# Optimization experiments

Measured on AMD Instinct MI355X. Metric: run time of the kernel, lower is better.

## Reference

```python
import jax, jax.numpy as jnp
import numpy as np

NUM_CHUNKS = 8
TOP_K = 2
IN_F = 4096
HID_F = 4096
OUT_F = 4096
B = 4096


def setup_inputs() -> dict:
    key = jax.random.key(0)
    k = jax.random.split(key, 5)
    cin = IN_F // NUM_CHUNKS    # 512
    cout = HID_F // NUM_CHUNKS  # 512
    s_in = 1.0 / np.sqrt(cin)
    s_fin = 1.0 / np.sqrt(cout * TOP_K)
    return {
        "x": jax.random.normal(k[0], (B, IN_F), dtype=jnp.float32),
        # stacked chunk-expert Linear params: y = x @ W + b
        "W_chunks": jax.random.uniform(k[1], (NUM_CHUNKS, cin, cout), jnp.float32, -s_in, s_in),
        "b_chunks": jax.random.uniform(k[2], (NUM_CHUNKS, cout), jnp.float32, -s_in, s_in),
        "W_final": jax.random.uniform(k[3], (cout * TOP_K, OUT_F), jnp.float32, -s_fin, s_fin),
        "b_final": jax.random.uniform(k[4], (OUT_F,), jnp.float32, -s_fin, s_fin),
    }


def reference(x, W_chunks, b_chunks, W_final, b_final):
    Bsz = x.shape[0]
    # split into chunks along feature dim: (B, num_chunks, chunk_in)
    xr = x.reshape(Bsz, NUM_CHUNKS, -1)
    # per-chunk activity = mean(|chunk|) over the whole batch (matches torch .abs().mean())
    activities = jnp.mean(jnp.abs(xr), axis=(0, 2))  # (num_chunks,)
    _, topk_idx = jax.lax.top_k(activities, TOP_K)    # descending, like torch.topk
    # gather selected chunks and their expert weights, run small GEMMs
    x_sel = xr[:, topk_idx, :]                        # (B, k, chunk_in)
    h = jnp.einsum('bkc,kcd->bkd', x_sel, W_chunks[topk_idx]) + b_chunks[topk_idx]
    h = h.reshape(Bsz, -1)                            # concat along feature dim
    out = h @ W_final + b_final                       # (B, out_features)
    return out
```

## Files before the change

kernel.cpp:

```cpp
#include <hip/hip_runtime.h>


typedef __bf16 bf16x8_t __attribute__((ext_vector_type(8)));
typedef float  f32x4_t  __attribute__((ext_vector_type(4)));
typedef unsigned short u16x4 __attribute__((ext_vector_type(4)));

__device__ inline unsigned short f2bf(float f) {
    __bf16 b = (__bf16)f;
    return __builtin_bit_cast(unsigned short, b);
}

__device__ inline void stage_glds(const unsigned short* gtile, int stride, int row0,
                                  unsigned short* lds, int lane) {
    const int r8 = lane >> 3;
    const int gg = (lane & 7) ^ r8;
    const unsigned short* gp = gtile + (size_t)(row0 + r8) * stride + gg * 8;
    unsigned short* lp = lds + row0 * 64;
    __builtin_amdgcn_global_load_lds((const __attribute__((address_space(1))) void*)gp,
                                     (__attribute__((address_space(3))) void*)lp,
                                     16, 0, 0);
}

__device__ inline bf16x8_t ldsfrag(const unsigned short* Ls, int row, int kb) {
    return *(const bf16x8_t*)(Ls + row * 64 + (((kb >> 3) ^ (row & 7)) * 8));
}

__global__ void fused_prep_kernel(const float* __restrict__ x, const float* __restrict__ Wc,
                                  const float* __restrict__ Wf, float* __restrict__ part,
                                  unsigned short* __restrict__ wct, unsigned short* __restrict__ wft) {
    const int b = blockIdx.x;
    const int tid = threadIdx.x;

    if (b < 512) {
        const int chunk = b & 7;
        const int rg = b >> 3;
        const int colf4 = tid & 127;
        const int rsub = tid >> 7;
        const float4* base = (const float4*)x + (size_t)chunk * 128 + colf4;
        float s = 0.f;
        #pragma unroll 4
        for (int i = 0; i < 32; ++i) {
            int row = rg * 64 + i * 2 + rsub;
            float4 v = base[(size_t)row * 1024];
            s += fabsf(v.x) + fabsf(v.y) + fabsf(v.z) + fabsf(v.w);
        }
        #pragma unroll
        for (int off = 32; off > 0; off >>= 1) s += __shfl_down(s, off, 64);
        __shared__ float wsum[4];
        if ((tid & 63) == 0) wsum[tid >> 6] = s;
        __syncthreads();
        if (tid == 0) part[chunk * 64 + rg] = wsum[0] + wsum[1] + wsum[2] + wsum[3];
        return;
    }

    __shared__ float tile[32][33];
    const int tx = tid & 31, ty = tid >> 5;
    const float* src; unsigned short* dst; int R, C, cb, rb;
    int jj = b - 512;
    if (jj < 4096) {
        src = Wf; dst = wft; R = 1024; C = 4096;
        cb = (jj & 127) * 32; rb = (jj >> 7) * 32;
    } else {
        jj -= 4096;
        int c = jj >> 8, t = jj & 255;
        src = Wc + (size_t)c * 262144;
        dst = wct + (size_t)c * 262144;
        R = 512; C = 512;
        cb = (t & 15) * 32; rb = (t >> 4) * 32;
    }
    #pragma unroll
    for (int i = 0; i < 4; ++i)
        tile[ty + i * 8][tx] = src[(size_t)(rb + ty + i * 8) * C + cb + tx];
    __syncthreads();
    {
        const int tx8  = tid & 7;
        const int ty32 = tid >> 3;
        u16x4 hv;
        #pragma unroll
        for (int j = 0; j < 4; ++j) hv[j] = f2bf(tile[tx8 * 4 + j][ty32]);
        *(u16x4*)(dst + (size_t)(cb + ty32) * R + rb + tx8 * 4) = hv;
    }
}

__global__ __launch_bounds__(256, 4)
void gemm1_kernel(const float* __restrict__ x, const unsigned short* __restrict__ wct,
                  const float* __restrict__ bc, const float* __restrict__ part,
                  unsigned short* __restrict__ h) {
    __shared__ __align__(16) unsigned char lds_raw[24576];
    unsigned short* As = (unsigned short*)lds_raw;
    unsigned short* Bs = (unsigned short*)(lds_raw + 8192);

    const int tid = threadIdx.x;
    const int wave = tid >> 6;
    const int lane = tid & 63;

    {
        float* sred = (float*)lds_raw;
        sred[tid] = part[tid];
        sred[tid + 256] = part[tid + 256];
        __syncthreads();
        float* act8 = (float*)(lds_raw + 2048);
        if (tid < 8) {
            float a = 0.f;
            #pragma unroll
            for (int k = 0; k < 64; ++k) a += sred[tid * 64 + k];
            act8[tid] = a;
        }
        __syncthreads();
    }
    int sel0, sel1;
    {
        const float* act8 = (const float*)(lds_raw + 2048);
        float v0 = -1e30f, v1 = -1e30f; int b0 = 0, b1 = 0;
        #pragma unroll
        for (int i = 0; i < 8; ++i) {
            float v = act8[i];
            if (v > v0) { v1 = v0; b1 = b0; v0 = v; b0 = i; }
            else if (v > v1) { v1 = v; b1 = i; }
        }
        sel0 = b0; sel1 = b1;
    }
    __syncthreads();

    const int z = blockIdx.z;
    const int idxz = z ? sel1 : sel0;
    const int m0 = blockIdx.x * 64;
    const int n0 = blockIdx.y * 128;
    const int wm = (wave >> 1) * 32;
    const int wn = (wave & 1) * 64;
    const int rl = lane & 15;
    const int quad = lane >> 4;

    const float* xtile = x + (size_t)m0 * 4096 + idxz * 512;
    const unsigned short* Btile = wct + (size_t)idxz * 262144 + (size_t)n0 * 512;

    f32x4_t acc[4][2] = {};
    const int ar = tid >> 2;
    const int aq = tid & 3;

    for (int k0 = 0; k0 < 512; k0 += 64) {
        #pragma unroll
        for (int s = wave; s < 16; s += 4)
            stage_glds(Btile + k0, 512, s * 8, Bs, lane);
        const float* gr = xtile + (size_t)ar * 4096 + k0;
        #pragma unroll
        for (int j = 0; j < 2; ++j) {
            int gg = aq * 2 + j;
            float4 a = *(const float4*)(gr + gg * 8);
            float4 c = *(const float4*)(gr + gg * 8 + 4);
            bf16x8_t v;
            v[0] = (__bf16)a.x; v[1] = (__bf16)a.y; v[2] = (__bf16)a.z; v[3] = (__bf16)a.w;
            v[4] = (__bf16)c.x; v[5] = (__bf16)c.y; v[6] = (__bf16)c.z; v[7] = (__bf16)c.w;
            *(bf16x8_t*)(As + ar * 64 + ((gg ^ (ar & 7)) * 8)) = v;
        }
        __syncthreads();
        #pragma unroll
        for (int kq = 0; kq < 2; ++kq) {
            const int kb = kq * 32 + quad * 8;
            bf16x8_t af[2], bfr[4];
            #pragma unroll
            for (int i = 0; i < 2; ++i) af[i]  = ldsfrag(As, wm + i * 16 + rl, kb);
            #pragma unroll
            for (int i = 0; i < 4; ++i) bfr[i] = ldsfrag(Bs, wn + i * 16 + rl, kb);
            #pragma unroll
            for (int ni = 0; ni < 4; ++ni)
                #pragma unroll
                for (int mi = 0; mi < 2; ++mi)
                    acc[ni][mi] = __builtin_amdgcn_mfma_f32_16x16x32_bf16(bfr[ni], af[mi], acc[ni][mi], 0, 0, 0);
        }
        __syncthreads();
    }

    const float* bias = bc + (size_t)idxz * 512;
    #pragma unroll
    for (int ni = 0; ni < 4; ++ni) {
        const int colb = n0 + wn + ni * 16 + quad * 4;
        f32x4_t bv4 = *(const f32x4_t*)(bias + colb);
        #pragma unroll
        for (int mi = 0; mi < 2; ++mi) {
            int row = m0 + wm + mi * 16 + rl;
            f32x4_t o = acc[ni][mi] + bv4;
            u16x4 hv;
            #pragma unroll
            for (int j = 0; j < 4; ++j) hv[j] = f2bf(o[j]);
            *(u16x4*)(h + (size_t)row * 1024 + z * 512 + colb) = hv;
        }
    }
}

__global__ __launch_bounds__(256, 4)
void gemm2_kernel(const unsigned short* __restrict__ h, const unsigned short* __restrict__ wft,
                  const float* __restrict__ bfin, float* __restrict__ out) {
    __shared__ __align__(16) unsigned short As[128 * 64];
    __shared__ __align__(16) unsigned short Bs[128 * 64];
    const int m0 = blockIdx.x * 128;
    const int n0 = blockIdx.y * 128;
    const int tid = threadIdx.x;
    const int wave = tid >> 6;
    const int lane = tid & 63;
    const int wm = (wave >> 1) * 64;
    const int wn = (wave & 1) * 64;
    const int rl = lane & 15;
    const int quad = lane >> 4;

    const unsigned short* Atile = h + (size_t)m0 * 1024;
    const unsigned short* Btile = wft + (size_t)n0 * 1024;

    f32x4_t acc[4][4] = {};

    for (int k0 = 0; k0 < 1024; k0 += 64) {
        #pragma unroll
        for (int s = wave; s < 32; s += 4) {
            if (s < 16) stage_glds(Atile + k0, 1024, s * 8, As, lane);
            else        stage_glds(Btile + k0, 1024, (s - 16) * 8, Bs, lane);
        }
        __syncthreads();
        #pragma unroll
        for (int kq = 0; kq < 2; ++kq) {
            const int kb = kq * 32 + quad * 8;
            bf16x8_t af[4], bfr[4];
            #pragma unroll
            for (int i = 0; i < 4; ++i) {
                af[i]  = ldsfrag(As, wm + i * 16 + rl, kb);
                bfr[i] = ldsfrag(Bs, wn + i * 16 + rl, kb);
            }
            #pragma unroll
            for (int mi = 0; mi < 4; ++mi)
                #pragma unroll
                for (int ni = 0; ni < 4; ++ni)
                    acc[mi][ni] = __builtin_amdgcn_mfma_f32_16x16x32_bf16(af[mi], bfr[ni], acc[mi][ni], 0, 0, 0);
        }
        __syncthreads();
    }

    const int row_l = quad * 4;
    float bv[4];
    #pragma unroll
    for (int ni = 0; ni < 4; ++ni) bv[ni] = bfin[n0 + wn + ni * 16 + rl];
    #pragma unroll
    for (int j = 0; j < 4; ++j) {
        #pragma unroll
        for (int mi = 0; mi < 4; ++mi) {
            int row = m0 + wm + mi * 16 + row_l + j;
            float* orow = out + (size_t)row * 4096 + n0 + wn + rl;
            #pragma unroll
            for (int ni = 0; ni < 4; ++ni)
                __builtin_nontemporal_store(acc[mi][ni][j] + bv[ni], &orow[ni * 16]);
        }
    }
}

extern "C" void kernel_launch(void* const* d_in, const int* in_sizes, int n_in,
                              void* d_out, int out_size, void* d_ws, size_t ws_size,
                              hipStream_t stream) {
    const float* x    = (const float*)d_in[0];
    const float* Wc   = (const float*)d_in[1];
    const float* bc   = (const float*)d_in[2];
    const float* Wf   = (const float*)d_in[3];
    const float* bfin = (const float*)d_in[4];
    float* out = (float*)d_out;

    float* part = (float*)d_ws;
    unsigned short* h   = (unsigned short*)((char*)d_ws + 4096);
    unsigned short* wct = h   + (size_t)4096 * 1024;
    unsigned short* wft = wct + (size_t)8 * 512 * 512;

    fused_prep_kernel<<<6656, 256, 0, stream>>>(x, Wc, Wf, part, wct, wft);
    gemm1_kernel<<<dim3(64, 4, 2), 256, 0, stream>>>(x, wct, bc, part, h);
    gemm2_kernel<<<dim3(32, 32, 1), 256, 0, stream>>>(h, wft, bfin, out);
}
```

Baseline: 188.3 us.

## Use 64x64 transpose tiles in prep and stage gemm2 epilogue through LDS

The weight-transpose part of the prep kernel now uses 64x64 tiles, so fewer blocks are launched and each thread does more work with wider writes. The gemm2 epilogue now writes bias-added accumulators into the reused LDS buffer in two halves, then stores full rows to global memory with 16-byte vector writes instead of scattered scalar nontemporal stores. The aim is coalesced output writes for the 64MB fp32 result, at the cost of extra LDS traffic, two more barriers per half, and plain rather than nontemporal stores.

New measurement: 183.1 us. 1.03x faster.

```diff
diff --git a/kernel.cpp b/kernel.cpp
--- a/kernel.cpp
+++ b/kernel.cpp
@@ -53,32 +53,38 @@
         return;
     }
 
-    __shared__ float tile[32][33];
-    const int tx = tid & 31, ty = tid >> 5;
+    __shared__ float tile[64][65];
     const float* src; unsigned short* dst; int R, C, cb, rb;
-    int jj = b - 512;
-    if (jj < 4096) {
+    if (b < 1536) {
+        int jj = b - 512;
         src = Wf; dst = wft; R = 1024; C = 4096;
-        cb = (jj & 127) * 32; rb = (jj >> 7) * 32;
+        cb = (jj & 63) * 64; rb = (jj >> 6) * 64;
     } else {
-        jj -= 4096;
-        int c = jj >> 8, t = jj & 255;
+        int jj = b - 1536;
+        int c = jj >> 6, t = jj & 63;
         src = Wc + (size_t)c * 262144;
         dst = wct + (size_t)c * 262144;
         R = 512; C = 512;
-        cb = (t & 15) * 32; rb = (t >> 4) * 32;
-    }
-    #pragma unroll
-    for (int i = 0; i < 4; ++i)
-        tile[ty + i * 8][tx] = src[(size_t)(rb + ty + i * 8) * C + cb + tx];
+        cb = (t & 7) * 64; rb = (t >> 3) * 64;
+    }
+    {
+        const int cx = tid & 63;
+        const int ry = tid >> 6;
+        #pragma unroll
+        for (int i = 0; i < 16; ++i)
+            tile[ry + i * 4][cx] = src[(size_t)(rb + ry + i * 4) * C + cb + cx];
+    }
     __syncthreads();
     {
-        const int tx8  = tid & 7;
-        const int ty32 = tid >> 3;
-        u16x4 hv;
-        #pragma unroll
-        for (int j = 0; j < 4; ++j) hv[j] = f2bf(tile[tx8 * 4 + j][ty32]);
-        *(u16x4*)(dst + (size_t)(cb + ty32) * R + rb + tx8 * 4) = hv;
+        const int c16 = tid & 15;
+        const int r16 = tid >> 4;
+        #pragma unroll
+        for (int p = 0; p < 4; ++p) {
+            u16x4 hv;
+            #pragma unroll
+            for (int j = 0; j < 4; ++j) hv[j] = f2bf(tile[c16 * 4 + j][r16 + p * 16]);
+            *(u16x4*)(dst + (size_t)(cb + r16 + p * 16) * R + rb + c16 * 4) = hv;
+        }
     }
 }
 
@@ -191,8 +197,9 @@
 __global__ __launch_bounds__(256, 4)
 void gemm2_kernel(const unsigned short* __restrict__ h, const unsigned short* __restrict__ wft,
                   const float* __restrict__ bfin, float* __restrict__ out) {
-    __shared__ __align__(16) unsigned short As[128 * 64];
-    __shared__ __align__(16) unsigned short Bs[128 * 64];
+    __shared__ __align__(16) unsigned short AsBs[2 * 8192];
+    unsigned short* As = AsBs;
+    unsigned short* Bs = AsBs + 8192;
     const int m0 = blockIdx.x * 128;
     const int n0 = blockIdx.y * 128;
     const int tid = threadIdx.x;
@@ -233,20 +240,33 @@
         __syncthreads();
     }
 
-    const int row_l = quad * 4;
+    float* ebuf = (float*)AsBs;
     float bv[4];
     #pragma unroll
     for (int ni = 0; ni < 4; ++ni) bv[ni] = bfin[n0 + wn + ni * 16 + rl];
+
     #pragma unroll
-    for (int j = 0; j < 4; ++j) {
-        #pragma unroll
-        for (int mi = 0; mi < 4; ++mi) {
-            int row = m0 + wm + mi * 16 + row_l + j;
-            float* orow = out + (size_t)row * 4096 + n0 + wn + rl;
-            #pragma unroll
-            for (int ni = 0; ni < 4; ++ni)
-                __builtin_nontemporal_store(acc[mi][ni][j] + bv[ni], &orow[ni * 16]);
-        }
+    for (int c = 0; c < 2; ++c) {
+        if ((wave >> 1) == c) {
+            #pragma unroll
+            for (int mi = 0; mi < 4; ++mi)
+                #pragma unroll
+                for (int ni = 0; ni < 4; ++ni)
+                    #pragma unroll
+                    for (int j = 0; j < 4; ++j)
+                        ebuf[(mi * 16 + quad * 4 + j) * 128 + wn + ni * 16 + rl]
+                            = acc[mi][ni][j] + bv[ni];
+        }
+        __syncthreads();
+        const int rr8 = tid >> 5;
+        const int c4  = tid & 31;
+        #pragma unroll
+        for (int i = 0; i < 8; ++i) {
+            int rr = i * 8 + rr8;
+            f32x4_t v = *(const f32x4_t*)(ebuf + rr * 128 + c4 * 4);
+            *(f32x4_t*)(out + (size_t)(m0 + c * 64 + rr) * 4096 + n0 + c4 * 4) = v;
+        }
+        __syncthreads();
     }
 }
 
@@ -265,7 +285,7 @@
     unsigned short* wct = h   + (size_t)4096 * 1024;
     unsigned short* wft = wct + (size_t)8 * 512 * 512;
 
-    fused_prep_kernel<<<6656, 256, 0, stream>>>(x, Wc, Wf, part, wct, wft);
+    fused_prep_kernel<<<2048, 256, 0, stream>>>(x, Wc, Wf, part, wct, wft);
     gemm1_kernel<<<dim3(64, 4, 2), 256, 0, stream>>>(x, wct, bc, part, h);
     gemm2_kernel<<<dim3(32, 32, 1), 256, 0, stream>>>(h, wft, bfin, out);
 }
```
